# Optimization experiments

Measured on AMD Instinct MI355X. Metric: run time of the kernel, lower is better.

Reference implementation:

```python
import jax, jax.numpy as jnp
import numpy as np

N_SAMPLES = 16384
IN_FEATURES = 2048
N_COMPONENTS = 512
MAX_CROSS_TERMS = 512
# With n_components=512, max_cross_terms=512: interaction_depth=2 -> only pairwise
# cross terms, and n_pairwise = min(512*511//2, 512) = 512 (the first 512 pairs in
# lexicographic (i, j), i<j order -- exactly what the chunked torch loops produce).
_pi, _pj = np.triu_indices(N_COMPONENTS, k=1)  # lexicographic row-major order
PAIR_I = jnp.asarray(_pi[:MAX_CROSS_TERMS])
PAIR_J = jnp.asarray(_pj[:MAX_CROSS_TERMS])
SQRT_EPS = 1e-8


def setup_inputs() -> dict:
    key = jax.random.key(0)
    k1, k2 = jax.random.split(key)
    X = jax.random.normal(k1, (N_SAMPLES, IN_FEATURES), dtype=jnp.float32)
    projection = jax.random.normal(k2, (IN_FEATURES, N_COMPONENTS), dtype=jnp.float32) / np.sqrt(N_COMPONENTS)
    return {"X": X, "projection": projection}


def reference(X, projection):
    # Random projection: [N, in] @ [in, C] -> [N, C]
    Xp = X @ projection
    n = X.shape[0]
    bias = jnp.ones((n, 1), dtype=X.dtype)                 # 'bias' chunk
    p1 = Xp                                                # power_1
    p2 = Xp * Xp                                           # power_2
    p3 = p2 * Xp                                           # power_3
    pairs = Xp[:, PAIR_I] * Xp[:, PAIR_J]                  # pairwise cross terms
    sq = jnp.sqrt(jnp.abs(Xp) + SQRT_EPS)                  # sqrt features
    # Feature layout matches torch offsets: bias | p1 | p2 | p3 | cross | sqrt
    return jnp.concatenate([bias, p1, p2, p3, pairs, sq], axis=1)  # [N, 2561]
```

## Files before the change

kernel.cpp:

```cpp
#include <hip/hip_runtime.h>
#include <hip/hip_bf16.h>
#include <math.h>


typedef __attribute__((ext_vector_type(4))) float f32x4;
typedef __attribute__((ext_vector_type(8))) short bf16x8;

#define MM 16384
#define NN 512
#define KK 2048
#define OUTW 2561

#define BM 128
#define BN 128
#define BK 32
#define NT (KK / BK)

__device__ __forceinline__ short f2bf(float x) {
  union { __hip_bfloat16 b; short s; } u;
  u.b = __float2bfloat16(x);
  return u.s;
}

__device__ __forceinline__ bf16x8 cvt8(f32x4 a, f32x4 b) {
  bf16x8 r;
  r[0] = f2bf(a[0]); r[1] = f2bf(a[1]); r[2] = f2bf(a[2]); r[3] = f2bf(a[3]);
  r[4] = f2bf(b[0]); r[5] = f2bf(b[1]); r[6] = f2bf(b[2]); r[7] = f2bf(b[3]);
  return r;
}

__device__ __forceinline__ void gl_lds16(const void* g, void* l) {
  __builtin_amdgcn_global_load_lds((const __attribute__((address_space(1))) unsigned int*)g,
                                   (__attribute__((address_space(3))) unsigned int*)l, 16, 0, 0);
}

__global__ __launch_bounds__(256) void prep_b(const float* __restrict__ P, short* __restrict__ Bt) {
  __shared__ float ts[64][65];
  const int tid = threadIdx.x;
  const int k0 = (blockIdx.x >> 3) * 64;
  const int n0 = (blockIdx.x & 7) * 64;
#pragma unroll
  for (int j = 0; j < 16; ++j) {
    int idx = j * 256 + tid;
    int kr = idx >> 6, nc = idx & 63;
    ts[kr][nc] = P[(size_t)(k0 + kr) * NN + n0 + nc];
  }
  __syncthreads();
#pragma unroll
  for (int j = 0; j < 16; ++j) {
    int idx = j * 256 + tid;
    int nr = idx >> 6, kc = idx & 63;
    Bt[(size_t)(n0 + nr) * KK + k0 + kc] = f2bf(ts[kc][nr]);
  }
}

__global__ __launch_bounds__(256) void gemm5(const float* __restrict__ X,
                                             const short* __restrict__ Bt,
                                             float* __restrict__ out) {
  __shared__ float Asf[3][BM * BK];
  __shared__ short Bsf[3][BN * BK];

  const int tid = threadIdx.x;
  const int wid = tid >> 6, lane = tid & 63;
  const int lrow = lane & 15, kh = lane >> 4;
  const int wr = wid >> 1, wc = wid & 1;

  const int bid = blockIdx.x;
  const int tile = (bid & 7) * 64 + (bid >> 3);
  const int m0 = (tile >> 2) * BM;
  const int n0 = (tile & 3) * BN;

  const float* aSrc[4];
  int aDst[4];
#pragma unroll
  for (int q = 0; q < 4; ++q) {
    int inst = wid * 4 + q;
    int row = inst * 8 + (lane >> 3);
    int slot = (lane & 7) ^ ((lane >> 3) & 7);
    aSrc[q] = X + (size_t)(m0 + row) * KK + slot * 4;
    aDst[q] = inst * 256;
  }
  const int kd = (lane & 3) ^ ((lane >> 3) & 3);
  const short* bSrc[2];
  int bDst[2];
#pragma unroll
  for (int p = 0; p < 2; ++p) {
    int R0 = (p * 4 + wid) * 16;
    bDst[p] = R0 * 32;
    bSrc[p] = Bt + (size_t)(n0 + R0 + (lane >> 2)) * KK + kd * 8;
  }

  int offA[4][2], offB[4];
#pragma unroll
  for (int m = 0; m < 4; ++m) {
    int r = wr * 64 + m * 16 + lrow;
    offA[m][0] = r * 32 + (((2 * kh) ^ (r & 7)) << 2);
    offA[m][1] = r * 32 + (((2 * kh + 1) ^ (r & 7)) << 2);
  }
#pragma unroll
  for (int n = 0; n < 4; ++n) {
    int r = wc * 64 + n * 16 + lrow;
    offB[n] = r * 32 + ((kh ^ ((r >> 1) & 3)) << 3);
  }

  f32x4 acc[4][4];
#pragma unroll
  for (int m = 0; m < 4; ++m)
#pragma unroll
    for (int n = 0; n < 4; ++n) acc[m][n] = (f32x4)0.0f;

  auto compute = [&](int b) {
    const float* ab = &Asf[b][0];
    const short* bb = &Bsf[b][0];
    bf16x8 af[4], bfr[4];
#pragma unroll
    for (int m = 0; m < 4; ++m) {
      f32x4 lo = *(const f32x4*)(ab + offA[m][0]);
      f32x4 hi = *(const f32x4*)(ab + offA[m][1]);
      af[m] = cvt8(lo, hi);
    }
#pragma unroll
    for (int n = 0; n < 4; ++n) bfr[n] = *(const bf16x8*)(bb + offB[n]);
#pragma unroll
    for (int m = 0; m < 4; ++m)
#pragma unroll
      for (int n = 0; n < 4; ++n)
        acc[m][n] = __builtin_amdgcn_mfma_f32_16x16x32_bf16(af[m], bfr[n], acc[m][n], 0, 0, 0);
  };

#pragma unroll
  for (int q = 0; q < 4; ++q) gl_lds16(aSrc[q], &Asf[0][aDst[q]]);
#pragma unroll
  for (int p = 0; p < 2; ++p) gl_lds16(bSrc[p], &Bsf[0][bDst[p]]);
#pragma unroll
  for (int q = 0; q < 4; ++q) gl_lds16(aSrc[q] + BK, &Asf[1][aDst[q]]);
#pragma unroll
  for (int p = 0; p < 2; ++p) gl_lds16(bSrc[p] + BK, &Bsf[1][bDst[p]]);

  int b0 = 0;
  for (int t = 0; t < NT - 2; ++t) {
    asm volatile("s_waitcnt vmcnt(6)" ::: "memory");
    __builtin_amdgcn_s_barrier();
    int b2 = b0 + 2; if (b2 >= 3) b2 -= 3;
#pragma unroll
    for (int q = 0; q < 4; ++q) gl_lds16(aSrc[q] + (size_t)(t + 2) * BK, &Asf[b2][aDst[q]]);
#pragma unroll
    for (int p = 0; p < 2; ++p) gl_lds16(bSrc[p] + (size_t)(t + 2) * BK, &Bsf[b2][bDst[p]]);
    compute(b0);
    b0 = (b0 == 2) ? 0 : b0 + 1;
  }
  asm volatile("s_waitcnt vmcnt(6)" ::: "memory");
  __builtin_amdgcn_s_barrier();
  compute(b0);
  b0 = (b0 == 2) ? 0 : b0 + 1;
  asm volatile("s_waitcnt vmcnt(0)" ::: "memory");
  __builtin_amdgcn_s_barrier();
  compute(b0);

#pragma unroll
  for (int m = 0; m < 4; ++m)
#pragma unroll
    for (int n = 0; n < 4; ++n)
#pragma unroll
      for (int r = 0; r < 4; ++r) {
        int row = m0 + wr * 64 + m * 16 + kh * 4 + r;
        int col = n0 + wc * 64 + n * 16 + lrow;
        out[(size_t)row * OUTW + 1 + col] = acc[m][n][r];
      }
}

__global__ __launch_bounds__(512) void epi_k(float* __restrict__ out) {
  const int r = blockIdx.x;
  const int c = threadIdx.x;
  float* row = out + (size_t)r * OUTW;
  __shared__ float s[NN];
  float xp = row[1 + c];
  s[c] = xp;
  __syncthreads();
  float p2 = xp * xp;
  float p3 = p2 * xp;
  float sq = sqrtf(fabsf(xp) + 1e-8f);
  float pr = (c < 511) ? s[0] * s[c + 1] : s[1] * s[2];
  if (c == 0) row[0] = 1.0f;
  row[513 + c] = p2;
  row[1025 + c] = p3;
  row[1537 + c] = pr;
  row[2049 + c] = sq;
}

#define FBM 128
#define FBN 128
#define FPAD 40

__global__ __launch_bounds__(256) void gemm_k(const float* __restrict__ A,
                                              const float* __restrict__ B,
                                              float* __restrict__ out) {
  __shared__ __align__(16) short Asf[FBM][FPAD];
  __shared__ __align__(16) short Bsf[FBN][FPAD];
  const int tid = threadIdx.x;
  const int bx = blockIdx.x;
  const int m0 = (bx >> 2) * FBM;
  const int n0 = (bx & 3) * FBN;
  const int wid = tid >> 6, lane = tid & 63;
  const int wr = wid >> 1, wc = wid & 1;
  const int lrow = lane & 15, kh = lane >> 4;
  f32x4 acc[4][4];
#pragma unroll
  for (int i = 0; i < 4; i++)
#pragma unroll
    for (int j = 0; j < 4; j++) acc[i][j] = (f32x4)0.0f;
  for (int k0 = 0; k0 < KK; k0 += BK) {
#pragma unroll
    for (int i = 0; i < 4; i++) {
      int fid = i * 256 + tid;
      int ar = fid >> 3, ac = (fid & 7) << 2;
      f32x4 v = *(const f32x4*)(A + (size_t)(m0 + ar) * KK + (k0 + ac));
      short h0 = f2bf(v[0]), h1 = f2bf(v[1]), h2 = f2bf(v[2]), h3 = f2bf(v[3]);
      Asf[ar][ac] = h0; Asf[ar][ac + 1] = h1; Asf[ar][ac + 2] = h2; Asf[ar][ac + 3] = h3;
    }
#pragma unroll
    for (int i = 0; i < 4; i++) {
      int fid = i * 256 + tid;
      int br = fid >> 5, bc = (fid & 31) << 2;
      f32x4 v = *(const f32x4*)(B + (size_t)(k0 + br) * NN + (n0 + bc));
#pragma unroll
      for (int j = 0; j < 4; j++) Bsf[bc + j][br] = f2bf(v[j]);
    }
    __syncthreads();
    bf16x8 af[4], bf[4];
#pragma unroll
    for (int m = 0; m < 4; m++) af[m] = *(const bf16x8*)&Asf[wr * 64 + m * 16 + lrow][kh * 8];
#pragma unroll
    for (int n = 0; n < 4; n++) bf[n] = *(const bf16x8*)&Bsf[wc * 64 + n * 16 + lrow][kh * 8];
#pragma unroll
    for (int m = 0; m < 4; m++)
#pragma unroll
      for (int n = 0; n < 4; n++)
        acc[m][n] = __builtin_amdgcn_mfma_f32_16x16x32_bf16(af[m], bf[n], acc[m][n], 0, 0, 0);
    __syncthreads();
  }
#pragma unroll
  for (int m = 0; m < 4; m++)
#pragma unroll
    for (int n = 0; n < 4; n++)
#pragma unroll
      for (int r = 0; r < 4; r++) {
        int row = m0 + wr * 64 + m * 16 + kh * 4 + r;
        int col = n0 + wc * 64 + n * 16 + lrow;
        out[(size_t)row * OUTW + 1 + col] = acc[m][n][r];
      }
}

extern "C" void kernel_launch(void* const* d_in, const int* in_sizes, int n_in,
                              void* d_out, int out_size, void* d_ws, size_t ws_size,
                              hipStream_t stream) {
  const float* X = (const float*)d_in[0];
  const float* P = (const float*)d_in[1];
  float* out = (float*)d_out;
  (void)in_sizes; (void)n_in; (void)out_size;

  if (ws_size >= (size_t)NN * KK * sizeof(short)) {
    short* Bt = (short*)d_ws;
    prep_b<<<dim3(256), dim3(256), 0, stream>>>(P, Bt);
    gemm5<<<dim3((MM / BM) * (NN / BN)), dim3(256), 0, stream>>>(X, Bt, out);
  } else {
    gemm_k<<<dim3(512), dim3(256), 0, stream>>>(X, P, out);
  }
  epi_k<<<dim3(MM), dim3(512), 0, stream>>>(out);
}
```

Before: 154.3 us.

## Stage A through registers with bf16 conversion before LDS write in GEMM

Replaces the direct global-to-LDS fp32 copy of X with register-staged loads that convert to bf16 once and write packed bf16 into swizzled LDS. The main loop becomes a two-register-set software pipeline over a triple LDS buffer. This halves LDS footprint and read traffic for A and removes the per-tile conversion that every wave previously repeated, at the cost of more registers and manual vmcnt/lgkmcnt bookkeeping.

```diff
diff --git a/kernel.cpp b/kernel.cpp
--- a/kernel.cpp
+++ b/kernel.cpp
@@ -54,11 +54,11 @@
   }
 }
 
-__global__ __launch_bounds__(256) void gemm5(const float* __restrict__ X,
+__global__ __launch_bounds__(256) void gemm6(const float* __restrict__ X,
                                              const short* __restrict__ Bt,
                                              float* __restrict__ out) {
-  __shared__ float Asf[3][BM * BK];
-  __shared__ short Bsf[3][BN * BK];
+  __shared__ short As[3][BM * BK];
+  __shared__ short Bs[3][BN * BK];
 
   const int tid = threadIdx.x;
   const int wid = tid >> 6, lane = tid & 63;
@@ -70,16 +70,12 @@
   const int m0 = (tile >> 2) * BM;
   const int n0 = (tile & 3) * BN;
 
-  const float* aSrc[4];
-  int aDst[4];
-#pragma unroll
-  for (int q = 0; q < 4; ++q) {
-    int inst = wid * 4 + q;
-    int row = inst * 8 + (lane >> 3);
-    int slot = (lane & 7) ^ ((lane >> 3) & 7);
-    aSrc[q] = X + (size_t)(m0 + row) * KK + slot * 4;
-    aDst[q] = inst * 256;
-  }
+  const int arow = tid >> 2, akq = tid & 3;
+  const float* aG0 = X + (size_t)(m0 + arow) * KK + akq * 8;
+  const float* aG1 = aG0 + (size_t)64 * KK;
+  const int aoff0 = arow * 32 + ((akq ^ ((arow >> 1) & 3)) << 3);
+  const int aoff1 = (64 + arow) * 32 + ((akq ^ (((64 + arow) >> 1) & 3)) << 3);
+
   const int kd = (lane & 3) ^ ((lane >> 3) & 3);
   const short* bSrc[2];
   int bDst[2];
@@ -90,37 +86,43 @@
     bSrc[p] = Bt + (size_t)(n0 + R0 + (lane >> 2)) * KK + kd * 8;
   }
 
-  int offA[4][2], offB[4];
-#pragma unroll
-  for (int m = 0; m < 4; ++m) {
-    int r = wr * 64 + m * 16 + lrow;
-    offA[m][0] = r * 32 + (((2 * kh) ^ (r & 7)) << 2);
-    offA[m][1] = r * 32 + (((2 * kh + 1) ^ (r & 7)) << 2);
-  }
-#pragma unroll
-  for (int n = 0; n < 4; ++n) {
-    int r = wc * 64 + n * 16 + lrow;
-    offB[n] = r * 32 + ((kh ^ ((r >> 1) & 3)) << 3);
-  }
-
   f32x4 acc[4][4];
 #pragma unroll
   for (int m = 0; m < 4; ++m)
 #pragma unroll
     for (int n = 0; n < 4; ++n) acc[m][n] = (f32x4)0.0f;
 
+  f32x4 s0[4], s1[4];
+
+  auto loadA = [&](f32x4 (&s)[4], int t) {
+    const float* p0 = aG0 + (size_t)t * BK;
+    const float* p1 = aG1 + (size_t)t * BK;
+    s[0] = *(const f32x4*)p0; s[1] = *(const f32x4*)(p0 + 4);
+    s[2] = *(const f32x4*)p1; s[3] = *(const f32x4*)(p1 + 4);
+  };
+  auto writeA = [&](f32x4 (&s)[4], int b) {
+    *(bf16x8*)&As[b][aoff0] = cvt8(s[0], s[1]);
+    *(bf16x8*)&As[b][aoff1] = cvt8(s[2], s[3]);
+  };
+  auto stageB = [&](int t, int b) {
+#pragma unroll
+    for (int p = 0; p < 2; ++p) gl_lds16(bSrc[p] + (size_t)t * BK, &Bs[b][bDst[p]]);
+  };
   auto compute = [&](int b) {
-    const float* ab = &Asf[b][0];
-    const short* bb = &Bsf[b][0];
+    const short* ab = &As[b][0];
+    const short* bb = &Bs[b][0];
+    const int sw = (lrow >> 1) & 3;
     bf16x8 af[4], bfr[4];
 #pragma unroll
     for (int m = 0; m < 4; ++m) {
-      f32x4 lo = *(const f32x4*)(ab + offA[m][0]);
-      f32x4 hi = *(const f32x4*)(ab + offA[m][1]);
-      af[m] = cvt8(lo, hi);
-    }
-#pragma unroll
-    for (int n = 0; n < 4; ++n) bfr[n] = *(const bf16x8*)(bb + offB[n]);
+      int r = wr * 64 + m * 16 + lrow;
+      af[m] = *(const bf16x8*)(ab + r * 32 + ((kh ^ sw) << 3));
+    }
+#pragma unroll
+    for (int n = 0; n < 4; ++n) {
+      int r = wc * 64 + n * 16 + lrow;
+      bfr[n] = *(const bf16x8*)(bb + r * 32 + ((kh ^ sw) << 3));
+    }
 #pragma unroll
     for (int m = 0; m < 4; ++m)
 #pragma unroll
@@ -128,34 +130,49 @@
         acc[m][n] = __builtin_amdgcn_mfma_f32_16x16x32_bf16(af[m], bfr[n], acc[m][n], 0, 0, 0);
   };
 
-#pragma unroll
-  for (int q = 0; q < 4; ++q) gl_lds16(aSrc[q], &Asf[0][aDst[q]]);
-#pragma unroll
-  for (int p = 0; p < 2; ++p) gl_lds16(bSrc[p], &Bsf[0][bDst[p]]);
-#pragma unroll
-  for (int q = 0; q < 4; ++q) gl_lds16(aSrc[q] + BK, &Asf[1][aDst[q]]);
-#pragma unroll
-  for (int p = 0; p < 2; ++p) gl_lds16(bSrc[p] + BK, &Bsf[1][bDst[p]]);
-
-  int b0 = 0;
-  for (int t = 0; t < NT - 2; ++t) {
-    asm volatile("s_waitcnt vmcnt(6)" ::: "memory");
+  loadA(s0, 0);
+  stageB(0, 0);
+  loadA(s1, 1);
+  stageB(1, 1);
+  asm volatile("s_waitcnt vmcnt(8)" ::: "memory");
+  writeA(s0, 0);
+  loadA(s0, 2);
+  asm volatile("s_waitcnt vmcnt(6)" ::: "memory");
+  writeA(s1, 1);
+  loadA(s1, 3);
+
+  for (int t = 0; t < NT - 4; t += 2) {
+    asm volatile("s_waitcnt vmcnt(6) lgkmcnt(0)" ::: "memory");
     __builtin_amdgcn_s_barrier();
-    int b2 = b0 + 2; if (b2 >= 3) b2 -= 3;
-#pragma unroll
-    for (int q = 0; q < 4; ++q) gl_lds16(aSrc[q] + (size_t)(t + 2) * BK, &Asf[b2][aDst[q]]);
-#pragma unroll
-    for (int p = 0; p < 2; ++p) gl_lds16(bSrc[p] + (size_t)(t + 2) * BK, &Bsf[b2][bDst[p]]);
-    compute(b0);
-    b0 = (b0 == 2) ? 0 : b0 + 1;
-  }
-  asm volatile("s_waitcnt vmcnt(6)" ::: "memory");
-  __builtin_amdgcn_s_barrier();
-  compute(b0);
-  b0 = (b0 == 2) ? 0 : b0 + 1;
-  asm volatile("s_waitcnt vmcnt(0)" ::: "memory");
-  __builtin_amdgcn_s_barrier();
-  compute(b0);
+    writeA(s0, (t + 2) % 3);
+    loadA(s0, t + 4);
+    stageB(t + 2, (t + 2) % 3);
+    compute(t % 3);
+
+    asm volatile("s_waitcnt vmcnt(6) lgkmcnt(0)" ::: "memory");
+    __builtin_amdgcn_s_barrier();
+    writeA(s1, (t + 3) % 3);
+    loadA(s1, t + 5);
+    stageB(t + 3, (t + 3) % 3);
+    compute((t + 1) % 3);
+  }
+
+  asm volatile("s_waitcnt vmcnt(6) lgkmcnt(0)" ::: "memory");
+  __builtin_amdgcn_s_barrier();
+  writeA(s0, (NT - 2) % 3);
+  stageB(NT - 2, (NT - 2) % 3);
+  compute((NT - 4) % 3);
+  asm volatile("s_waitcnt vmcnt(2) lgkmcnt(0)" ::: "memory");
+  __builtin_amdgcn_s_barrier();
+  writeA(s1, (NT - 1) % 3);
+  stageB(NT - 1, (NT - 1) % 3);
+  compute((NT - 3) % 3);
+  asm volatile("s_waitcnt vmcnt(2) lgkmcnt(0)" ::: "memory");
+  __builtin_amdgcn_s_barrier();
+  compute((NT - 2) % 3);
+  asm volatile("s_waitcnt vmcnt(0) lgkmcnt(0)" ::: "memory");
+  __builtin_amdgcn_s_barrier();
+  compute((NT - 1) % 3);
 
 #pragma unroll
   for (int m = 0; m < 4; ++m)
@@ -262,7 +279,7 @@
   if (ws_size >= (size_t)NN * KK * sizeof(short)) {
     short* Bt = (short*)d_ws;
     prep_b<<<dim3(256), dim3(256), 0, stream>>>(P, Bt);
-    gemm5<<<dim3((MM / BM) * (NN / BN)), dim3(256), 0, stream>>>(X, Bt, out);
+    gemm6<<<dim3((MM / BM) * (NN / BN)), dim3(256), 0, stream>>>(X, Bt, out);
   } else {
     gemm_k<<<dim3(512), dim3(256), 0, stream>>>(X, P, out);
   }
```

Measured after the change: 135.9 us. -11.9%, faster.
